# Kernel tuning notes

Measured on AMD Instinct MI355X. Metric: run time of the kernel, lower is better.

The kernel has to match this reference:

```python
import jax, jax.numpy as jnp
import numpy as np

V, D = 100000, 512
B, K = 32768, 10


def setup_inputs() -> dict:
    key = jax.random.key(0)
    k1, k2, k3, k4, k5 = jax.random.split(key, 5)
    return {
        "center_ids": jax.random.randint(k1, (B,), 0, V),
        "context_ids": jax.random.randint(k2, (B,), 0, V),
        "neg_context_ids": jax.random.randint(k3, (B, K), 0, V),
        "center_emb": jax.random.normal(k4, (V, D), dtype=jnp.float32) * (1.0 / D),
        "context_emb": jax.random.normal(k5, (V, D), dtype=jnp.float32) * (1.0 / D),
    }


def reference(center_ids, context_ids, neg_context_ids, center_emb, context_emb):
    cv = center_emb[center_ids]            # [B, D]
    ctx = context_emb[context_ids]         # [B, D]
    score = jnp.sum(cv * ctx, axis=1)      # [B]
    score = jnp.clip(score, -10.0, 10.0)
    pos_loss = -jax.nn.log_sigmoid(score)  # [B]
    neg = context_emb[neg_context_ids]     # [B, K, D]
    neg_score = jnp.einsum("bkd,bd->bk", neg, cv)  # [B, K]
    neg_score = jnp.clip(neg_score, -10.0, 10.0)
    neg_loss = -jnp.sum(jax.nn.log_sigmoid(-neg_score), axis=1)  # [B]
    return jnp.mean(pos_loss + neg_loss)
```

## Files before the change

kernel.cpp:

```cpp
#include <hip/hip_runtime.h>
#include <math.h>

#define NB 32768
#define NK 10
#define ND 512
#define WPB 4
#define GRID (NB / WPB)

__global__ __launch_bounds__(256) void sgns_main(
    const int*   __restrict__ center_ids,
    const int*   __restrict__ context_ids,
    const int*   __restrict__ neg_ids,
    const float* __restrict__ center_emb,
    const float* __restrict__ context_emb,
    float*       __restrict__ partials)
{
    const int tid  = threadIdx.x;
    const int lane = tid & 63;
    const int wave = tid >> 6;
    const int grp  = lane >> 4;
    const int li   = lane & 15;
    const int b    = blockIdx.x * WPB + wave;

    const int ctx_id = context_ids[b];
    int rid[3];
#pragma unroll
    for (int r = 0; r < 3; ++r) {
        const int s = r * 4 + grp;
        rid[r] = (s == 0 || s == 11) ? ctx_id : neg_ids[b * NK + (s - 1)];
    }

    const float4* cvp = (const float4*)(center_emb  + (size_t)center_ids[b] * ND) + li;
    const float4* rpA = (const float4*)(context_emb + (size_t)rid[0] * ND) + li;
    const float4* rpB = (const float4*)(context_emb + (size_t)rid[1] * ND) + li;
    const float4* rpC = (const float4*)(context_emb + (size_t)rid[2] * ND) + li;

    __builtin_amdgcn_sched_barrier(0);

    float4 cv[8], ra[8], rb[8], rc[8];
#pragma unroll
    for (int j = 0; j < 8; ++j) cv[j] = cvp[16 * j];
#pragma unroll
    for (int j = 0; j < 8; ++j) ra[j] = rpA[16 * j];
#pragma unroll
    for (int j = 0; j < 8; ++j) rb[j] = rpB[16 * j];
#pragma unroll
    for (int j = 0; j < 8; ++j) rc[j] = rpC[16 * j];

    __builtin_amdgcn_sched_barrier(0);

    float lacc = 0.0f;

    {
        float p = 0.0f;
#pragma unroll
        for (int j = 0; j < 8; ++j)
            p += cv[j].x * ra[j].x + cv[j].y * ra[j].y
               + cv[j].z * ra[j].z + cv[j].w * ra[j].w;
#pragma unroll
        for (int off = 1; off < 16; off <<= 1) p += __shfl_xor(p, off, 64);
        float t = fminf(fmaxf(p, -10.0f), 10.0f);
        t = (grp == 0) ? -t : t;
        lacc += __logf(1.0f + __expf(t));
    }

    {
        float p = 0.0f;
#pragma unroll
        for (int j = 0; j < 8; ++j)
            p += cv[j].x * rb[j].x + cv[j].y * rb[j].y
               + cv[j].z * rb[j].z + cv[j].w * rb[j].w;
#pragma unroll
        for (int off = 1; off < 16; off <<= 1) p += __shfl_xor(p, off, 64);
        float t = fminf(fmaxf(p, -10.0f), 10.0f);
        lacc += __logf(1.0f + __expf(t));
    }

    {
        float p = 0.0f;
#pragma unroll
        for (int j = 0; j < 8; ++j)
            p += cv[j].x * rc[j].x + cv[j].y * rc[j].y
               + cv[j].z * rc[j].z + cv[j].w * rc[j].w;
#pragma unroll
        for (int off = 1; off < 16; off <<= 1) p += __shfl_xor(p, off, 64);
        float t = fminf(fmaxf(p, -10.0f), 10.0f);
        float l = __logf(1.0f + __expf(t));
        lacc += (grp == 3) ? 0.0f : l;
    }

    lacc += __shfl_xor(lacc, 16, 64);
    lacc += __shfl_xor(lacc, 32, 64);

    __shared__ float ls[WPB];
    if (lane == 0) ls[wave] = lacc;
    __syncthreads();
    if (tid == 0)
        partials[blockIdx.x] = ls[0] + ls[1] + ls[2] + ls[3];
}

__global__ __launch_bounds__(1024) void sgns_finish(
    const float* __restrict__ partials, float* __restrict__ out, int n)
{
    __shared__ float ls[1024];
    float s = 0.0f;
    for (int i = threadIdx.x; i < n; i += 1024) s += partials[i];
    ls[threadIdx.x] = s;
    __syncthreads();
    for (int w = 512; w > 0; w >>= 1) {
        if (threadIdx.x < w) ls[threadIdx.x] += ls[threadIdx.x + w];
        __syncthreads();
    }
    if (threadIdx.x == 0) out[0] = ls[0] * (1.0f / (float)NB);
}

extern "C" void kernel_launch(void* const* d_in, const int* in_sizes, int n_in,
                              void* d_out, int out_size, void* d_ws, size_t ws_size,
                              hipStream_t stream) {
    const int*   center_ids  = (const int*)d_in[0];
    const int*   context_ids = (const int*)d_in[1];
    const int*   neg_ids     = (const int*)d_in[2];
    const float* center_emb  = (const float*)d_in[3];
    const float* context_emb = (const float*)d_in[4];
    float* out      = (float*)d_out;
    float* partials = (float*)d_ws;

    sgns_main<<<GRID, 256, 0, stream>>>(center_ids, context_ids, neg_ids,
                                        center_emb, context_emb, partials);
    sgns_finish<<<1, 1024, 0, stream>>>(partials, out, GRID);
}
```

Measured before the change: 116.8 us.

## Bucket-sort context lookups by row id to improve cache reuse of embeddings

```diff
diff --git a/kernel.cpp b/kernel.cpp
--- a/kernel.cpp
+++ b/kernel.cpp
@@ -3,25 +3,152 @@
 
 #define NB 32768
 #define NK 10
+#define NV 100000
 #define ND 512
-#define WPB 4
-#define GRID (NB / WPB)
-
-__global__ __launch_bounds__(256) void sgns_main(
+#define NSLOT 11
+#define NTASK (NB * NSLOT)
+#define BSHIFT 6
+#define NBUCKET_PAD 2048
+#define NXCD 8
+
+#define REC_OFF  0
+#define LOSS_OFF (NTASK * 8)
+#define HIST_OFF (LOSS_OFF + NTASK * 4)
+#define OFFS_OFF (HIST_OFF + NBUCKET_PAD * 4)
+#define PART_OFF (OFFS_OFF + NBUCKET_PAD * 4)
+#define WS_NEED  (PART_OFF + 2048 * 4)
+
+__global__ void zero_hist(unsigned* hist) {
+    int i = blockIdx.x * blockDim.x + threadIdx.x;
+    if (i < NBUCKET_PAD) hist[i] = 0;
+}
+
+__global__ __launch_bounds__(256) void hist_kernel(
+    const int* __restrict__ context_ids, const int* __restrict__ neg_ids,
+    unsigned* __restrict__ hist)
+{
+    int t = blockIdx.x * blockDim.x + threadIdx.x;
+    if (t >= NTASK) return;
+    int b = t / NSLOT, slot = t - b * NSLOT;
+    int id = (slot == 0) ? context_ids[b] : neg_ids[b * NK + slot - 1];
+    atomicAdd(&hist[id >> BSHIFT], 1u);
+}
+
+__global__ __launch_bounds__(1024) void scan_kernel(
+    const unsigned* __restrict__ hist, unsigned* __restrict__ offs)
+{
+    __shared__ unsigned s[1024];
+    const int t = threadIdx.x;
+    const unsigned a = hist[2 * t], b = hist[2 * t + 1];
+    s[t] = a + b;
+    __syncthreads();
+    for (int off = 1; off < 1024; off <<= 1) {
+        unsigned v = (t >= off) ? s[t - off] : 0u;
+        __syncthreads();
+        s[t] += v;
+        __syncthreads();
+    }
+    const unsigned excl = (t > 0) ? s[t - 1] : 0u;
+    offs[2 * t]     = excl;
+    offs[2 * t + 1] = excl + a;
+}
+
+__global__ __launch_bounds__(256) void scatter_kernel(
+    const int* __restrict__ context_ids, const int* __restrict__ neg_ids,
+    unsigned* __restrict__ offs, uint2* __restrict__ rec)
+{
+    int t = blockIdx.x * blockDim.x + threadIdx.x;
+    if (t >= NTASK) return;
+    int b = t / NSLOT, slot = t - b * NSLOT;
+    int id = (slot == 0) ? context_ids[b] : neg_ids[b * NK + slot - 1];
+    unsigned pos = atomicAdd(&offs[id >> BSHIFT], 1u);
+    rec[pos] = make_uint2((unsigned)id, ((unsigned)b << 4) | (unsigned)slot);
+}
+
+__global__ __launch_bounds__(256) void dot_kernel(
+    const uint2* __restrict__ rec,
     const int*   __restrict__ center_ids,
-    const int*   __restrict__ context_ids,
-    const int*   __restrict__ neg_ids,
     const float* __restrict__ center_emb,
     const float* __restrict__ context_emb,
-    float*       __restrict__ partials)
-{
-    const int tid  = threadIdx.x;
-    const int lane = tid & 63;
-    const int wave = tid >> 6;
-    const int grp  = lane >> 4;
-    const int li   = lane & 15;
-    const int b    = blockIdx.x * WPB + wave;
-
+    float*       __restrict__ loss)
+{
+    const int nwg = NTASK / 16;
+    const int cpx = nwg / NXCD;
+    const int lb  = (blockIdx.x % NXCD) * cpx + blockIdx.x / NXCD;
+
+    const int tid = threadIdx.x;
+    const int li  = tid & 15;
+    const int g   = lb * 16 + (tid >> 4);
+
+    const uint2 r  = rec[g];
+    const int   id   = (int)r.x;
+    const int   b    = (int)(r.y >> 4);
+    const int   slot = (int)(r.y & 15u);
+
+    const float4* cp  = (const float4*)(context_emb + (size_t)id * ND) + li;
+    const float4* cvp = (const float4*)(center_emb + (size_t)center_ids[b] * ND) + li;
+
+    __builtin_amdgcn_sched_barrier(0);
+    float4 cx[8], cv[8];
+#pragma unroll
+    for (int j = 0; j < 8; ++j) cx[j] = cp[16 * j];
+#pragma unroll
+    for (int j = 0; j < 8; ++j) cv[j] = cvp[16 * j];
+    __builtin_amdgcn_sched_barrier(0);
+
+    float p = 0.0f;
+#pragma unroll
+    for (int j = 0; j < 8; ++j)
+        p += cv[j].x * cx[j].x + cv[j].y * cx[j].y
+           + cv[j].z * cx[j].z + cv[j].w * cx[j].w;
+#pragma unroll
+    for (int off = 1; off < 16; off <<= 1) p += __shfl_xor(p, off, 64);
+
+    if (li == 0) {
+        float t = fminf(fmaxf(p, -10.0f), 10.0f);
+        t = (slot == 0) ? -t : t;
+        loss[b * NSLOT + slot] = __logf(1.0f + __expf(t));
+    }
+}
+
+__global__ __launch_bounds__(256) void reduce1(
+    const float* __restrict__ loss, float* __restrict__ part)
+{
+    __shared__ float ls[256];
+    ls[threadIdx.x] = loss[blockIdx.x * 256 + threadIdx.x];
+    __syncthreads();
+    for (int w = 128; w > 0; w >>= 1) {
+        if (threadIdx.x < w) ls[threadIdx.x] += ls[threadIdx.x + w];
+        __syncthreads();
+    }
+    if (threadIdx.x == 0) part[blockIdx.x] = ls[0];
+}
+
+__global__ __launch_bounds__(1024) void reduce2(
+    const float* __restrict__ part, float* __restrict__ out, int n, float scale)
+{
+    __shared__ float ls[1024];
+    float s = 0.0f;
+    for (int i = threadIdx.x; i < n; i += 1024) s += part[i];
+    ls[threadIdx.x] = s;
+    __syncthreads();
+    for (int w = 512; w > 0; w >>= 1) {
+        if (threadIdx.x < w) ls[threadIdx.x] += ls[threadIdx.x + w];
+        __syncthreads();
+    }
+    if (threadIdx.x == 0) out[0] = ls[0] * scale;
+}
+
+#define WPB 4
+#define FGRID (NB / WPB)
+__global__ __launch_bounds__(256) void sgns_fallback(
+    const int* __restrict__ center_ids, const int* __restrict__ context_ids,
+    const int* __restrict__ neg_ids, const float* __restrict__ center_emb,
+    const float* __restrict__ context_emb, float* __restrict__ partials)
+{
+    const int tid = threadIdx.x, lane = tid & 63, wave = tid >> 6;
+    const int grp = lane >> 4, li = lane & 15;
+    const int b = blockIdx.x * WPB + wave;
     const int ctx_id = context_ids[b];
     int rid[3];
 #pragma unroll
@@ -29,14 +156,10 @@
         const int s = r * 4 + grp;
         rid[r] = (s == 0 || s == 11) ? ctx_id : neg_ids[b * NK + (s - 1)];
     }
-
     const float4* cvp = (const float4*)(center_emb  + (size_t)center_ids[b] * ND) + li;
     const float4* rpA = (const float4*)(context_emb + (size_t)rid[0] * ND) + li;
     const float4* rpB = (const float4*)(context_emb + (size_t)rid[1] * ND) + li;
     const float4* rpC = (const float4*)(context_emb + (size_t)rid[2] * ND) + li;
-
-    __builtin_amdgcn_sched_barrier(0);
-
     float4 cv[8], ra[8], rb[8], rc[8];
 #pragma unroll
     for (int j = 0; j < 8; ++j) cv[j] = cvp[16 * j];
@@ -46,72 +169,45 @@
     for (int j = 0; j < 8; ++j) rb[j] = rpB[16 * j];
 #pragma unroll
     for (int j = 0; j < 8; ++j) rc[j] = rpC[16 * j];
-
-    __builtin_amdgcn_sched_barrier(0);
-
     float lacc = 0.0f;
-
     {
         float p = 0.0f;
 #pragma unroll
         for (int j = 0; j < 8; ++j)
-            p += cv[j].x * ra[j].x + cv[j].y * ra[j].y
-               + cv[j].z * ra[j].z + cv[j].w * ra[j].w;
+            p += cv[j].x*ra[j].x + cv[j].y*ra[j].y + cv[j].z*ra[j].z + cv[j].w*ra[j].w;
 #pragma unroll
         for (int off = 1; off < 16; off <<= 1) p += __shfl_xor(p, off, 64);
         float t = fminf(fmaxf(p, -10.0f), 10.0f);
         t = (grp == 0) ? -t : t;
         lacc += __logf(1.0f + __expf(t));
     }
-
     {
         float p = 0.0f;
 #pragma unroll
         for (int j = 0; j < 8; ++j)
-            p += cv[j].x * rb[j].x + cv[j].y * rb[j].y
-               + cv[j].z * rb[j].z + cv[j].w * rb[j].w;
+            p += cv[j].x*rb[j].x + cv[j].y*rb[j].y + cv[j].z*rb[j].z + cv[j].w*rb[j].w;
 #pragma unroll
         for (int off = 1; off < 16; off <<= 1) p += __shfl_xor(p, off, 64);
         float t = fminf(fmaxf(p, -10.0f), 10.0f);
         lacc += __logf(1.0f + __expf(t));
     }
-
     {
         float p = 0.0f;
 #pragma unroll
         for (int j = 0; j < 8; ++j)
-            p += cv[j].x * rc[j].x + cv[j].y * rc[j].y
-               + cv[j].z * rc[j].z + cv[j].w * rc[j].w;
+            p += cv[j].x*rc[j].x + cv[j].y*rc[j].y + cv[j].z*rc[j].z + cv[j].w*rc[j].w;
 #pragma unroll
         for (int off = 1; off < 16; off <<= 1) p += __shfl_xor(p, off, 64);
         float t = fminf(fmaxf(p, -10.0f), 10.0f);
         float l = __logf(1.0f + __expf(t));
         lacc += (grp == 3) ? 0.0f : l;
     }
-
     lacc += __shfl_xor(lacc, 16, 64);
     lacc += __shfl_xor(lacc, 32, 64);
-
     __shared__ float ls[WPB];
     if (lane == 0) ls[wave] = lacc;
     __syncthreads();
-    if (tid == 0)
-        partials[blockIdx.x] = ls[0] + ls[1] + ls[2] + ls[3];
-}
-
-__global__ __launch_bounds__(1024) void sgns_finish(
-    const float* __restrict__ partials, float* __restrict__ out, int n)
-{
-    __shared__ float ls[1024];
-    float s = 0.0f;
-    for (int i = threadIdx.x; i < n; i += 1024) s += partials[i];
-    ls[threadIdx.x] = s;
-    __syncthreads();
-    for (int w = 512; w > 0; w >>= 1) {
-        if (threadIdx.x < w) ls[threadIdx.x] += ls[threadIdx.x + w];
-        __syncthreads();
-    }
-    if (threadIdx.x == 0) out[0] = ls[0] * (1.0f / (float)NB);
+    if (tid == 0) partials[blockIdx.x] = ls[0] + ls[1] + ls[2] + ls[3];
 }
 
 extern "C" void kernel_launch(void* const* d_in, const int* in_sizes, int n_in,
@@ -122,10 +218,27 @@
     const int*   neg_ids     = (const int*)d_in[2];
     const float* center_emb  = (const float*)d_in[3];
     const float* context_emb = (const float*)d_in[4];
-    float* out      = (float*)d_out;
-    float* partials = (float*)d_ws;
-
-    sgns_main<<<GRID, 256, 0, stream>>>(center_ids, context_ids, neg_ids,
-                                        center_emb, context_emb, partials);
-    sgns_finish<<<1, 1024, 0, stream>>>(partials, out, GRID);
-}
+    float* out = (float*)d_out;
+    char*  ws  = (char*)d_ws;
+
+    if (ws_size >= (size_t)WS_NEED) {
+        uint2*    rec  = (uint2*)(ws + REC_OFF);
+        float*    loss = (float*)(ws + LOSS_OFF);
+        unsigned* hist = (unsigned*)(ws + HIST_OFF);
+        unsigned* offs = (unsigned*)(ws + OFFS_OFF);
+        float*    part = (float*)(ws + PART_OFF);
+
+        zero_hist<<<NBUCKET_PAD / 256, 256, 0, stream>>>(hist);
+        hist_kernel<<<(NTASK + 255) / 256, 256, 0, stream>>>(context_ids, neg_ids, hist);
+        scan_kernel<<<1, 1024, 0, stream>>>(hist, offs);
+        scatter_kernel<<<(NTASK + 255) / 256, 256, 0, stream>>>(context_ids, neg_ids, offs, rec);
+        dot_kernel<<<NTASK / 16, 256, 0, stream>>>(rec, center_ids, center_emb, context_emb, loss);
+        reduce1<<<NTASK / 256, 256, 0, stream>>>(loss, part);
+        reduce2<<<1, 1024, 0, stream>>>(part, out, NTASK / 256, 1.0f / (float)NB);
+    } else {
+        float* partials = (float*)d_ws;
+        sgns_fallback<<<FGRID, 256, 0, stream>>>(center_ids, context_ids, neg_ids,
+                                                 center_emb, context_emb, partials);
+        reduce2<<<1, 1024, 0, stream>>>(partials, out, FGRID, 1.0f / (float)NB);
+    }
+}
```

After: 253.6 us. 2.17x slower.
